# Kernel tuning notes

Hardware: AMD Instinct MI355X
Metric: run time of the kernel (lower is better)

Reference implementation:

```python
import jax, jax.numpy as jnp
import numpy as np

N, E, G = 20000, 320000, 64
IN_DIM, HID, HEADS, NCLS = 512, 256, 2, 10
EPS = 1e-5
SLOPE = 0.2


def setup_inputs() -> dict:
    key = jax.random.key(0)
    ks = jax.random.split(key, 24)
    s = 0.02
    inp = {
        "feat": jax.random.normal(ks[0], (N, IN_DIM), jnp.float32),
        "src": jax.random.randint(ks[1], (E,), 0, N, jnp.int32),
        "dst": jax.random.randint(ks[2], (E,), 0, N, jnp.int32),
        "graph_ids": jnp.sort(jax.random.randint(ks[3], (N,), 0, G, jnp.int32)),
        # GATv2Conv params (fc_src, fc_dst, attn)
        "W_src": jax.random.normal(ks[4], (IN_DIM, HEADS * HID), jnp.float32) * s,
        "b_src": jnp.zeros((HEADS * HID,), jnp.float32),
        "W_dst": jax.random.normal(ks[5], (IN_DIM, HEADS * HID), jnp.float32) * s,
        "b_dst": jnp.zeros((HEADS * HID,), jnp.float32),
        "attn": jax.random.normal(ks[6], (HEADS, HID), jnp.float32) * s,
        # skip_lin: input_dim -> 2*hidden
        "W_skip": jax.random.normal(ks[7], (IN_DIM, 2 * HID), jnp.float32) * s,
        "b_skip": jnp.zeros((2 * HID,), jnp.float32),
        # bn1 affine
        "gamma": jnp.ones((2 * HID,), jnp.float32),
        "beta": jnp.zeros((2 * HID,), jnp.float32),
        # dim_reducer
        "W_red": jax.random.normal(ks[8], (2 * HID, HID), jnp.float32) * s,
        "b_red": jnp.zeros((HID,), jnp.float32),
        # attention-pool gate Linear(hidden, 1)
        "w_gate": jax.random.normal(ks[9], (HID, 1), jnp.float32) * s,
        "b_gate": jnp.zeros((1,), jnp.float32),
        # classifier MLP
        "W1": jax.random.normal(ks[10], (HID, HID // 2), jnp.float32) * s,
        "b1": jnp.zeros((HID // 2,), jnp.float32),
        "W2": jax.random.normal(ks[11], (HID // 2, NCLS), jnp.float32) * s,
        "b2": jnp.zeros((NCLS,), jnp.float32),
    }
    return inp


def _gatv2(feat, src, dst, W_src, b_src, W_dst, b_dst, attn):
    # feat_src/feat_dst: [N, H, D]
    fs = (feat @ W_src + b_src).reshape(N, HEADS, HID)
    fd = (feat @ W_dst + b_dst).reshape(N, HEADS, HID)
    fs_e = fs[src]                               # [E, H, D]
    m = jax.nn.leaky_relu(fs_e + fd[dst], SLOPE)  # [E, H, D]
    e = jnp.einsum("ehd,hd->eh", m, attn)         # [E, H]
    # edge softmax grouped by destination node
    e_max = jax.ops.segment_max(e, dst, num_segments=N)          # [N, H]
    e_exp = jnp.exp(e - e_max[dst])                               # [E, H]
    denom = jax.ops.segment_sum(e_exp, dst, num_segments=N)      # [N, H]
    alpha = e_exp / denom[dst]                                    # [E, H]
    out = jax.ops.segment_sum(alpha[:, :, None] * fs_e, dst, num_segments=N)
    return out  # [N, H, D]; zero rows for zero in-degree nodes


def reference(feat, src, dst, graph_ids, W_src, b_src, W_dst, b_dst, attn,
              W_skip, b_skip, gamma, beta, W_red, b_red, w_gate, b_gate,
              W1, b1, W2, b2):
    h1 = jax.nn.elu(_gatv2(feat, src, dst, W_src, b_src, W_dst, b_dst, attn))
    h1 = h1.reshape(N, HEADS * HID)
    h1 = h1 + (feat @ W_skip + b_skip)
    # BatchNorm1d (training-mode batch statistics, biased variance)
    mu = jnp.mean(h1, axis=0)
    var = jnp.mean((h1 - mu) ** 2, axis=0)
    h1 = (h1 - mu) * jax.lax.rsqrt(var + EPS) * gamma + beta
    hr = h1 @ W_red + b_red                      # [N, HID]
    # GlobalAttentionPooling: segment softmax of gate scores over each graph
    gate = hr @ w_gate + b_gate                  # [N, 1]
    g_max = jax.ops.segment_max(gate, graph_ids, num_segments=G)
    g_exp = jnp.exp(gate - g_max[graph_ids])
    g_den = jax.ops.segment_sum(g_exp, graph_ids, num_segments=G)
    a = g_exp / g_den[graph_ids]                 # [N, 1]
    h_g = jax.ops.segment_sum(a * hr, graph_ids, num_segments=G)  # [G, HID]
    # classifier (dropout = identity at inference)
    return jax.nn.relu(h_g @ W1 + b1) @ W2 + b2  # [G, NCLS]
```

## Files before the change

kernel.cpp:

```cpp
#include <hip/hip_runtime.h>
#include <math.h>

#define N_NODES 20000
#define N_EDGES 320000
#define N_GRAPH 64
#define IN_DIM  512
#define HID     256
#define F2      512
#define EPS_BN  1e-5f
#define SLOPE   0.2f
#define SCAN_BLOCKS 79
#define N_RT    157
#define RT_PAD  20096

#define SF_BLOCKS   5024
#define SW_BLOCKS   1024
#define INIT_BLOCKS 79
#define HIST_BLOCKS 1250
#define PREP_BLOCKS (SF_BLOCKS + SW_BLOCKS + INIT_BLOCKS + HIST_BLOCKS)
#define TRIPLE_BLOCKS 1920

typedef unsigned short u16;
typedef __attribute__((ext_vector_type(8))) short bf16x8;
typedef __attribute__((ext_vector_type(4))) float floatx4;
typedef _Float16 f16;
typedef __attribute__((ext_vector_type(2))) f16 f16x2;

__device__ __forceinline__ u16 bf_hi(float x) {
    unsigned int u = __float_as_uint(x);
    return (u16)((u + 0x7fffu + ((u >> 16) & 1u)) >> 16);
}
__device__ __forceinline__ float bf_val(u16 h) {
    return __uint_as_float((unsigned int)h << 16);
}
__device__ __forceinline__ f16x2 h2_from_u32(unsigned int u) {
    return __builtin_bit_cast(f16x2, u);
}
__device__ __forceinline__ unsigned int u32_from_h2(f16x2 h) {
    return __builtin_bit_cast(unsigned int, h);
}

__device__ __forceinline__ void gload16(const u16* g, u16* l) {
    __builtin_amdgcn_global_load_lds(
        (const __attribute__((address_space(1))) void*)g,
        (__attribute__((address_space(3))) void*)l, 16, 0, 0);
}

__global__ __launch_bounds__(256) void prep_kernel(
    const float* __restrict__ feat, u16* __restrict__ Fhi,
    const float* __restrict__ Ws, const float* __restrict__ Wd,
    const float* __restrict__ Wk, const float* __restrict__ Wr,
    u16* __restrict__ Whi, u16* __restrict__ Wlo,
    const int* __restrict__ dst, int* __restrict__ counts,
    int* __restrict__ cursor,
    float* __restrict__ stats, float* __restrict__ h_gnum,
    float* __restrict__ gden) {
    __shared__ float t[32][33];
    int b = blockIdx.x;
    int tid = threadIdx.x;
    if (b < SF_BLOCKS) {
        int i = b * 256 + tid;
        size_t base = (size_t)i * 8;
        if (i >= N_NODES * IN_DIM / 8) {
            *(uint4*)(Fhi + base) = make_uint4(0, 0, 0, 0);
            return;
        }
        float4 x0 = *(const float4*)(feat + base);
        float4 x1 = *(const float4*)(feat + base + 4);
        float xs[8] = {x0.x, x0.y, x0.z, x0.w, x1.x, x1.y, x1.z, x1.w};
        union { u16 s[8]; uint4 v; } h;
#pragma unroll
        for (int j = 0; j < 8; j++) h.s[j] = bf_hi(xs[j]);
        *(uint4*)(Fhi + base) = h.v;
    } else if (b < SF_BLOCKS + SW_BLOCKS) {
        int bb = b - SF_BLOCKS;
        int kx = bb & 15, ny = (bb >> 4) & 15, w = bb >> 8;
        int ncols = (w == 3) ? 256 : 512;
        int n0 = ny * 32;
        if (n0 >= ncols) return;
        const float* W = (w == 0) ? Ws : ((w == 1) ? Wd : ((w == 2) ? Wk : Wr));
        size_t obase = (size_t)w * 512 * 512;
        int k0 = kx * 32;
        int tx = tid & 31, ty = tid >> 5;
#pragma unroll
        for (int i = 0; i < 4; i++)
            t[ty * 4 + i][tx] = W[(size_t)(k0 + ty * 4 + i) * ncols + n0 + tx];
        __syncthreads();
#pragma unroll
        for (int i = 0; i < 4; i++) {
            float x = t[tx][ty * 4 + i];
            u16 hh = bf_hi(x);
            size_t o = obase + (size_t)(n0 + ty * 4 + i) * 512 + k0 + tx;
            Whi[o] = hh;
            Wlo[o] = bf_hi(x - bf_val(hh));
        }
    } else if (b < SF_BLOCKS + SW_BLOCKS + INIT_BLOCKS) {
        int i = (b - SF_BLOCKS - SW_BLOCKS) * 256 + tid;
        if (i < N_NODES) cursor[i] = 0;
        if (i < 1024) stats[i] = 0.f;
        if (i < N_GRAPH * HID) h_gnum[i] = 0.f;
        if (i < N_GRAPH) gden[i] = 0.f;
    } else {
        int e = (b - SF_BLOCKS - SW_BLOCKS - INIT_BLOCKS) * 256 + tid;
        if (e < N_EDGES) atomicAdd(&counts[dst[e]], 1);
    }
}

__global__ __launch_bounds__(256) void gemm_mfma_triple(
    const u16* __restrict__ Fhi, const u16* __restrict__ Wthi,
    const float* __restrict__ b_src, const float* __restrict__ b_dst,
    const float* __restrict__ b_skip,
    u16* __restrict__ FS16, u16* __restrict__ FD16,
    u16* __restrict__ h1hi, u16* __restrict__ h1lo,
    const int* __restrict__ counts, int* __restrict__ row_ptr,
    int* __restrict__ bsum) {
    __shared__ u16 S[2][2][8192];
    int b = blockIdx.x;
    int tid = threadIdx.x;
    if (b >= TRIPLE_BLOCKS) {
        int* buf = (int*)&S[0][0][0];
        int bb = b - TRIPLE_BLOCKS;
        int i = bb * 256 + tid;
        buf[tid] = (i < N_NODES) ? counts[i] : 0;
        __syncthreads();
        for (int off = 1; off < 256; off <<= 1) {
            int t = (tid >= off) ? buf[tid - off] : 0;
            __syncthreads();
            buf[tid] += t;
            __syncthreads();
        }
        if (i < N_NODES) row_ptr[i + 1] = buf[tid];
        if (tid == 255) bsum[bb] = buf[255];
        return;
    }
    int xcd = b & 7, slot = b >> 3;
    int rt = (slot / 12) * 8 + xcd;
    if (rt >= N_RT) return;
    int cw = slot % 12;
    int w_idx = cw >> 2;
    int col0 = (cw & 3) * 128;
    int row0 = rt * 128;
    int lane = tid & 63, wave = tid >> 6;
    int wm = (wave & 1) * 64, wn = (wave >> 1) * 64;
    int quad = lane >> 4, l16 = lane & 15;

    int lrow = lane >> 3;
    int kswz = ((lane & 7) ^ lrow) << 3;
    const u16* aS = Fhi + (size_t)(row0 + wave * 32 + lrow) * 512 + kswz;
    const u16* bS = Wthi + (size_t)w_idx * 512 * 512 +
                    (size_t)(col0 + wave * 32 + lrow) * 512 + kswz;

#define STAGE(buf, kk)                                                        \
    do {                                                                      \
        gload16(aS + (size_t)(kk) * 64,         &S[buf][0][(wave * 4 + 0) * 512]); \
        gload16(bS + (size_t)(kk) * 64,         &S[buf][1][(wave * 4 + 0) * 512]); \
        gload16(aS + 4096 + (size_t)(kk) * 64,  &S[buf][0][(wave * 4 + 1) * 512]); \
        gload16(bS + 4096 + (size_t)(kk) * 64,  &S[buf][1][(wave * 4 + 1) * 512]); \
        gload16(aS + 8192 + (size_t)(kk) * 64,  &S[buf][0][(wave * 4 + 2) * 512]); \
        gload16(bS + 8192 + (size_t)(kk) * 64,  &S[buf][1][(wave * 4 + 2) * 512]); \
        gload16(aS + 12288 + (size_t)(kk) * 64, &S[buf][0][(wave * 4 + 3) * 512]); \
        gload16(bS + 12288 + (size_t)(kk) * 64, &S[buf][1][(wave * 4 + 3) * 512]); \
    } while (0)

    int kx8 = (l16 & 7) << 3;
    int oS0 = (quad * 8) ^ kx8;
    int offA = (wm + l16) * 64;
    int offB = (wn + l16) * 64;

    floatx4 acc[4][4];
#pragma unroll
    for (int i = 0; i < 4; i++)
#pragma unroll
        for (int j = 0; j < 4; j++) acc[i][j] = (floatx4){0.f, 0.f, 0.f, 0.f};

    STAGE(0, 0);
    __syncthreads();

#pragma unroll
    for (int kk = 0; kk < 8; kk++) {
        if (kk < 7) STAGE((kk + 1) & 1, kk + 1);
        const u16* A = &S[kk & 1][0][0];
        const u16* B = &S[kk & 1][1][0];
        bf16x8 bv[4][2];
#pragma unroll
        for (int nt = 0; nt < 4; nt++) {
            bv[nt][0] = *(const bf16x8*)&B[offB + nt * 1024 + oS0];
            bv[nt][1] = *(const bf16x8*)&B[offB + nt * 1024 + (oS0 ^ 32)];
        }
#pragma unroll
        for (int mt = 0; mt < 4; mt++) {
            bf16x8 a0 = *(const bf16x8*)&A[offA + mt * 1024 + oS0];
            bf16x8 a1 = *(const bf16x8*)&A[offA + mt * 1024 + (oS0 ^ 32)];
#pragma unroll
            for (int nt = 0; nt < 4; nt++) {
                acc[mt][nt] = __builtin_amdgcn_mfma_f32_16x16x32_bf16(
                    bv[nt][0], a0, acc[mt][nt], 0, 0, 0);
                acc[mt][nt] = __builtin_amdgcn_mfma_f32_16x16x32_bf16(
                    bv[nt][1], a1, acc[mt][nt], 0, 0, 0);
            }
        }
        __syncthreads();
    }
#undef STAGE

    const float* bias = (w_idx == 0) ? b_src : ((w_idx == 1) ? b_dst : b_skip);
    float4 b4[4];
#pragma unroll
    for (int wt = 0; wt < 4; wt++)
        b4[wt] = *(const float4*)(bias + col0 + wn + wt * 16 + quad * 4);

    u16* C = &S[0][0][0];
#pragma unroll
    for (int ft = 0; ft < 4; ft++) {
        int r = wm + ft * 16 + l16;
        int rx = r & 7;
#pragma unroll
        for (int wt = 0; wt < 4; wt++) {
            int cb = wn + wt * 16 + quad * 4;
            int off = r * 128 + (((cb >> 3) ^ rx) << 3) + (cb & 4);
            float v0 = acc[ft][wt][0] + b4[wt].x;
            float v1 = acc[ft][wt][1] + b4[wt].y;
            float v2 = acc[ft][wt][2] + b4[wt].z;
            float v3 = acc[ft][wt][3] + b4[wt].w;
            if (w_idx <= 1) {
                f16x2 p0; p0[0] = (f16)v0; p0[1] = (f16)v1;
                f16x2 p1; p1[0] = (f16)v2; p1[1] = (f16)v3;
                uint2 wv;
                wv.x = u32_from_h2(p0);
                wv.y = u32_from_h2(p1);
                *(uint2*)&C[off] = wv;
            } else {
                u16 h0 = bf_hi(v0), h1_ = bf_hi(v1), h2 = bf_hi(v2), h3 = bf_hi(v3);
                uint2 wv;
                wv.x = (unsigned)h0 | ((unsigned)h1_ << 16);
                wv.y = (unsigned)h2 | ((unsigned)h3 << 16);
                *(uint2*)&C[off] = wv;
                uint2 lv;
                lv.x = (unsigned)bf_hi(v0 - bf_val(h0)) | ((unsigned)bf_hi(v1 - bf_val(h1_)) << 16);
                lv.y = (unsigned)bf_hi(v2 - bf_val(h2)) | ((unsigned)bf_hi(v3 - bf_val(h3)) << 16);
                *(uint2*)&C[16384 + off] = lv;
            }
        }
    }
    __syncthreads();
    {
        int tr = tid >> 4;
        int tc = tid & 15;
        u16* outp = (w_idx == 0) ? FS16 : ((w_idx == 1) ? FD16 : h1hi);
#pragma unroll
        for (int i = 0; i < 8; i++) {
            int r = i * 16 + tr;
            int m = row0 + r;
            int loff = r * 128 + ((tc ^ (r & 7)) << 3);
            uint4 v = *(const uint4*)&C[loff];
            if (m < N_NODES) {
                *(uint4*)(outp + (size_t)m * 512 + col0 + tc * 8) = v;
                if (w_idx == 2) {
                    uint4 vl = *(const uint4*)&C[16384 + loff];
                    *(uint4*)(h1lo + (size_t)m * 512 + col0 + tc * 8) = vl;
                }
            }
        }
    }
}

__global__ __launch_bounds__(256) void scan_fixup_kernel(
    const int* __restrict__ bsum, int* __restrict__ row_ptr) {
    __shared__ int red[256];
    int b = blockIdx.x, tid = threadIdx.x;
    red[tid] = (tid < b) ? bsum[tid] : 0;
    __syncthreads();
    for (int off = 128; off > 0; off >>= 1) {
        if (tid < off) red[tid] += red[tid + off];
        __syncthreads();
    }
    int offset = red[0];
    int i = b * 256 + tid;
    if (i < N_NODES) row_ptr[i + 1] += offset;
    if (b == 0 && tid == 0) row_ptr[0] = 0;
}

__global__ void scatter_kernel(const int* __restrict__ src, const int* __restrict__ dst,
                               const int* __restrict__ row_ptr,
                               int* __restrict__ cursor, int* __restrict__ csr_src) {
    int e = blockIdx.x * blockDim.x + threadIdx.x;
    if (e < N_EDGES) {
        int d = dst[e];
        int pos = atomicAdd(&cursor[d], 1);
        csr_src[row_ptr[d] + pos] = src[e];
    }
}

__global__ __launch_bounds__(256) void edge_fused_kernel(
    const u16* __restrict__ FS16, const u16* __restrict__ FD16,
    const float* __restrict__ attn, const int* __restrict__ csr_src,
    const int* __restrict__ row_ptr,
    u16* __restrict__ h1hi, u16* __restrict__ h1lo) {
    int tid = threadIdx.x;
    int lane = tid & 63, wave = tid >> 6;
    int n = blockIdx.x * 4 + wave;
    int beg = row_ptr[n], end = row_ptr[n + 1];

    f16x2 fd2[4], aw2[4];
    {
        uint4 q = *(const uint4*)(FD16 + (size_t)n * 512 + 8 * lane);
        fd2[0] = h2_from_u32(q.x); fd2[1] = h2_from_u32(q.y);
        fd2[2] = h2_from_u32(q.z); fd2[3] = h2_from_u32(q.w);
        float4 a0 = *(const float4*)(attn + 8 * lane);
        float4 a1 = *(const float4*)(attn + 8 * lane + 4);
        aw2[0][0] = (f16)a0.x; aw2[0][1] = (f16)a0.y;
        aw2[1][0] = (f16)a0.z; aw2[1][1] = (f16)a0.w;
        aw2[2][0] = (f16)a1.x; aw2[2][1] = (f16)a1.y;
        aw2[3][0] = (f16)a1.z; aw2[3][1] = (f16)a1.w;
    }

    const f16x2 sl2 = {(f16)SLOPE, (f16)SLOPE};
    float acc[8] = {0.f, 0.f, 0.f, 0.f, 0.f, 0.f, 0.f, 0.f};
    float den = 0.f;
    const u16* FSb = FS16 + 8 * lane;

    int j = beg;
    for (; j + 3 < end; j += 4) {
        int s0 = csr_src[j];
        int s1 = csr_src[j + 1];
        int s2 = csr_src[j + 2];
        int s3 = csr_src[j + 3];
        uint4 q0 = *(const uint4*)(FSb + (size_t)s0 * 512);
        uint4 q1 = *(const uint4*)(FSb + (size_t)s1 * 512);
        uint4 q2 = *(const uint4*)(FSb + (size_t)s2 * 512);
        uint4 q3 = *(const uint4*)(FSb + (size_t)s3 * 512);
        f16x2 f0[4], f1[4], f2[4], f3[4];
        f0[0] = h2_from_u32(q0.x); f0[1] = h2_from_u32(q0.y);
        f0[2] = h2_from_u32(q0.z); f0[3] = h2_from_u32(q0.w);
        f1[0] = h2_from_u32(q1.x); f1[1] = h2_from_u32(q1.y);
        f1[2] = h2_from_u32(q1.z); f1[3] = h2_from_u32(q1.w);
        f2[0] = h2_from_u32(q2.x); f2[1] = h2_from_u32(q2.y);
        f2[2] = h2_from_u32(q2.z); f2[3] = h2_from_u32(q2.w);
        f3[0] = h2_from_u32(q3.x); f3[1] = h2_from_u32(q3.y);
        f3[2] = h2_from_u32(q3.z); f3[3] = h2_from_u32(q3.w);
        float p0 = 0.f, p1 = 0.f, p2 = 0.f, p3 = 0.f;
#pragma unroll
        for (int k = 0; k < 4; k++) {
            f16x2 sm0 = f0[k] + fd2[k];
            p0 = __builtin_amdgcn_fdot2(
                __builtin_elementwise_max(sm0, sm0 * sl2), aw2[k], p0, false);
            f16x2 sm1 = f1[k] + fd2[k];
            p1 = __builtin_amdgcn_fdot2(
                __builtin_elementwise_max(sm1, sm1 * sl2), aw2[k], p1, false);
            f16x2 sm2 = f2[k] + fd2[k];
            p2 = __builtin_amdgcn_fdot2(
                __builtin_elementwise_max(sm2, sm2 * sl2), aw2[k], p2, false);
            f16x2 sm3 = f3[k] + fd2[k];
            p3 = __builtin_amdgcn_fdot2(
                __builtin_elementwise_max(sm3, sm3 * sl2), aw2[k], p3, false);
        }
#pragma unroll
        for (int off = 16; off > 0; off >>= 1) {
            p0 += __shfl_xor(p0, off, 64);
            p1 += __shfl_xor(p1, off, 64);
            p2 += __shfl_xor(p2, off, 64);
            p3 += __shfl_xor(p3, off, 64);
        }
        float e0 = __expf(p0);
        float e1 = __expf(p1);
        float e2 = __expf(p2);
        float e3 = __expf(p3);
#pragma unroll
        for (int k = 0; k < 4; k++) {
            acc[2 * k]     += e0 * (float)f0[k][0] + e1 * (float)f1[k][0]
                            + e2 * (float)f2[k][0] + e3 * (float)f3[k][0];
            acc[2 * k + 1] += e0 * (float)f0[k][1] + e1 * (float)f1[k][1]
                            + e2 * (float)f2[k][1] + e3 * (float)f3[k][1];
        }
        den += (e0 + e1) + (e2 + e3);
    }
    for (; j < end; j++) {
        int s = csr_src[j];
        uint4 q = *(const uint4*)(FSb + (size_t)s * 512);
        f16x2 f2v[4];
        f2v[0] = h2_from_u32(q.x); f2v[1] = h2_from_u32(q.y);
        f2v[2] = h2_from_u32(q.z); f2v[3] = h2_from_u32(q.w);
        float p = 0.f;
#pragma unroll
        for (int k = 0; k < 4; k++) {
            f16x2 sm = f2v[k] + fd2[k];
            p = __builtin_amdgcn_fdot2(
                __builtin_elementwise_max(sm, sm * sl2), aw2[k], p, false);
        }
#pragma unroll
        for (int off = 16; off > 0; off >>= 1) p += __shfl_xor(p, off, 64);
        float ex = __expf(p);
#pragma unroll
        for (int k = 0; k < 4; k++) {
            acc[2 * k]     += ex * (float)f2v[k][0];
            acc[2 * k + 1] += ex * (float)f2v[k][1];
        }
        den += ex;
    }

    float inv = den > 0.f ? 1.f / den : 0.f;
    size_t base = (size_t)n * 512 + 8 * lane;
    union { u16 s[8]; uint4 v; } qh, ql;
    qh.v = *(const uint4*)(h1hi + base);
    ql.v = *(const uint4*)(h1lo + base);
#pragma unroll
    for (int k = 0; k < 8; k++) {
        float skip = bf_val(qh.s[k]) + bf_val(ql.s[k]);
        float x = acc[k] * inv;
        x = x > 0.f ? x : expm1f(x);
        float y = x + skip;
        u16 hh = bf_hi(y);
        qh.s[k] = hh;
        ql.s[k] = bf_hi(y - bf_val(hh));
    }
    *(uint4*)(h1hi + base) = qh.v;
    *(uint4*)(h1lo + base) = ql.v;
}

__global__ __launch_bounds__(256) void bn_stats_kernel(const u16* __restrict__ h1hi,
                                                       float* __restrict__ stats,
                                                       int rows_per_block) {
    int tid = threadIdx.x;
    int r0 = blockIdx.x * rows_per_block;
    int r1 = min(r0 + rows_per_block, N_NODES);
    float s0 = 0.f, q0 = 0.f, s1 = 0.f, q1 = 0.f;
    for (int r = r0; r < r1; r++) {
        float a = bf_val(h1hi[(size_t)r * F2 + tid]);
        float b = bf_val(h1hi[(size_t)r * F2 + 256 + tid]);
        s0 += a; q0 += a * a;
        s1 += b; q1 += b * b;
    }
    atomicAdd(&stats[tid], s0);
    atomicAdd(&stats[256 + tid], s1);
    atomicAdd(&stats[512 + tid], q0);
    atomicAdd(&stats[512 + 256 + tid], q1);
}

__global__ __launch_bounds__(256) void bn_fold_kernel(
    const float* __restrict__ stats, const float* __restrict__ gamma,
    const float* __restrict__ beta,
    const u16* __restrict__ Whi3, const u16* __restrict__ Wlo3,
    const float* __restrict__ b_red,
    u16* __restrict__ Wphi, u16* __restrict__ Wplo, float* __restrict__ bias2) {
    __shared__ float sScale[512], sShift[512];
    __shared__ float red[256];
    int n = blockIdx.x, tid = threadIdx.x;
    for (int c = tid; c < 512; c += 256) {
        float mu = stats[c] / (float)N_NODES;
        float var = stats[512 + c] / (float)N_NODES - mu * mu;
        float sc = gamma[c] * rsqrtf(var + EPS_BN);
        sScale[c] = sc;
        sShift[c] = beta[c] - mu * sc;
    }
    __syncthreads();
    float part = 0.f;
    for (int k = tid; k < 512; k += 256) {
        size_t o = (size_t)n * 512 + k;
        float w = bf_val(Whi3[o]) + bf_val(Wlo3[o]);
        part += sShift[k] * w;
        float wp = w * sScale[k];
        u16 hh = bf_hi(wp);
        Wphi[o] = hh;
        Wplo[o] = bf_hi(wp - bf_val(hh));
    }
    red[tid] = part; __syncthreads();
    for (int off = 128; off > 0; off >>= 1) {
        if (tid < off) red[tid] += red[tid + off];
        __syncthreads();
    }
    if (tid == 0) bias2[n] = b_red[n] + red[0];
}

__global__ __launch_bounds__(512) void gemm_mfma_red(
    const u16* __restrict__ Ahi, const u16* __restrict__ Alo,
    const u16* __restrict__ Bhi, const u16* __restrict__ Blo,
    const float* __restrict__ bias2, const float* __restrict__ wg,
    const int* __restrict__ gids,
    float* __restrict__ h_gnum, float* __restrict__ gden) {
    __shared__ u16 AsHi[128 * 40];
    __shared__ u16 AsLo[128 * 40];
    __shared__ float gacc[128];
    __shared__ float pacc[8][256];
    __shared__ float dacc[8];
    int tid = threadIdx.x;
    int row0 = blockIdx.x * 128;
    int lane = tid & 63, wave = tid >> 6;
    int wm = (wave & 1) * 64, wn = (wave >> 1) * 64;
    int quad = lane >> 4, l16 = lane & 15;

    if (tid < 128) gacc[tid] = 0.f;
    if (tid < 8) dacc[tid] = 0.f;
    for (int i = tid; i < 8 * 256; i += 512) ((float*)pacc)[i] = 0.f;

    int sr = tid >> 2, sh = (tid & 3) * 8;
    int grow = row0 + sr;
    bool ok = grow < N_NODES;
    u16* sH = &AsHi[sr * 40 + sh];
    u16* sL = &AsLo[sr * 40 + sh];

    const u16* bPh[4];
    const u16* bPl[4];
#pragma unroll
    for (int nt = 0; nt < 4; nt++) {
        size_t o = (size_t)(wn + nt * 16 + l16) * 512 + quad * 8;
        bPh[nt] = Bhi + o;
        bPl[nt] = Blo + o;
    }

    floatx4 acc[4][4];
#pragma unroll
    for (int i = 0; i < 4; i++)
#pragma unroll
        for (int j = 0; j < 4; j++) acc[i][j] = (floatx4){0.f, 0.f, 0.f, 0.f};

    for (int k0 = 0; k0 < 512; k0 += 32) {
        uint4 h0 = make_uint4(0, 0, 0, 0), l0 = h0;
        if (ok) {
            h0 = *(const uint4*)(Ahi + (size_t)grow * 512 + k0 + sh);
            l0 = *(const uint4*)(Alo + (size_t)grow * 512 + k0 + sh);
        }
        union { uint4 u; bf16x8 v; } bh[4], bl[4];
#pragma unroll
        for (int nt = 0; nt < 4; nt++) {
            bh[nt].u = *(const uint4*)(bPh[nt] + k0);
            bl[nt].u = *(const uint4*)(bPl[nt] + k0);
        }
        __syncthreads();
        *(uint4*)sH = h0;
        *(uint4*)sL = l0;
        __syncthreads();
#pragma unroll
        for (int mt = 0; mt < 4; mt++) {
            int me = (wm + mt * 16 + l16) * 40 + quad * 8;
            bf16x8 ah = *(const bf16x8*)&AsHi[me];
            bf16x8 al = *(const bf16x8*)&AsLo[me];
#pragma unroll
            for (int nt = 0; nt < 4; nt++) {
                acc[mt][nt] = __builtin_amdgcn_mfma_f32_16x16x32_bf16(bh[nt].v, ah, acc[mt][nt], 0, 0, 0);
                acc[mt][nt] = __builtin_amdgcn_mfma_f32_16x16x32_bf16(bl[nt].v, ah, acc[mt][nt], 0, 0, 0);
                acc[mt][nt] = __builtin_amdgcn_mfma_f32_16x16x32_bf16(bh[nt].v, al, acc[mt][nt], 0, 0, 0);
            }
        }
    }

    float4 b4[4], w4[4];
#pragma unroll
    for (int wt = 0; wt < 4; wt++) {
        int nb = wn + wt * 16 + quad * 4;
        b4[wt] = *(const float4*)(bias2 + nb);
        w4[wt] = *(const float4*)(wg + nb);
    }
#pragma unroll
    for (int ft = 0; ft < 4; ft++) {
        int r = wm + ft * 16 + l16;
        float g = 0.f;
#pragma unroll
        for (int wt = 0; wt < 4; wt++) {
            float4 v;
            v.x = acc[ft][wt][0] + b4[wt].x;
            v.y = acc[ft][wt][1] + b4[wt].y;
            v.z = acc[ft][wt][2] + b4[wt].z;
            v.w = acc[ft][wt][3] + b4[wt].w;
            g += v.x * w4[wt].x + v.y * w4[wt].y + v.z * w4[wt].z + v.w * w4[wt].w;
        }
        g += __shfl_xor(g, 16, 64);
        g += __shfl_xor(g, 32, 64);
        if (quad == 0) atomicAdd(&gacc[r], g);
    }
    __syncthreads();

    int g0 = gids[row0];
#pragma unroll
    for (int ft = 0; ft < 4; ft++) {
        int r = wm + ft * 16 + l16;
        int m = row0 + r;
        if (m >= N_NODES) continue;
        float wgt = __expf(gacc[r]);
        int d = gids[m] - g0;
        if (d < 8) {
            if ((wave >> 1) == 0 && quad == 0) atomicAdd(&dacc[d], wgt);
#pragma unroll
            for (int wt = 0; wt < 4; wt++) {
                int nb = wn + wt * 16 + quad * 4;
                atomicAdd(&pacc[d][nb + 0], wgt * (acc[ft][wt][0] + b4[wt].x));
                atomicAdd(&pacc[d][nb + 1], wgt * (acc[ft][wt][1] + b4[wt].y));
                atomicAdd(&pacc[d][nb + 2], wgt * (acc[ft][wt][2] + b4[wt].z));
                atomicAdd(&pacc[d][nb + 3], wgt * (acc[ft][wt][3] + b4[wt].w));
            }
        } else {
            int gg = gids[m];
            if ((wave >> 1) == 0 && quad == 0) atomicAdd(&gden[gg], wgt);
#pragma unroll
            for (int wt = 0; wt < 4; wt++) {
                int nb = wn + wt * 16 + quad * 4;
                atomicAdd(&h_gnum[gg * HID + nb + 0], wgt * (acc[ft][wt][0] + b4[wt].x));
                atomicAdd(&h_gnum[gg * HID + nb + 1], wgt * (acc[ft][wt][1] + b4[wt].y));
                atomicAdd(&h_gnum[gg * HID + nb + 2], wgt * (acc[ft][wt][2] + b4[wt].z));
                atomicAdd(&h_gnum[gg * HID + nb + 3], wgt * (acc[ft][wt][3] + b4[wt].w));
            }
        }
    }
    __syncthreads();

    int mlast = min(row0 + 127, N_NODES - 1);
    int span = gids[mlast] - g0;
    if (span > 7) span = 7;
    for (int i = tid; i < (span + 1) * 256; i += 512) {
        int d = i >> 8, c = i & 255;
        atomicAdd(&h_gnum[(g0 + d) * HID + c], pacc[d][c]);
    }
    if (tid <= span) atomicAdd(&gden[g0 + tid], dacc[tid]);
}

__global__ __launch_bounds__(128) void classifier_kernel(
    const float* __restrict__ h_gnum, const float* __restrict__ gden,
    const float* __restrict__ W1, const float* __restrict__ b1,
    const float* __restrict__ W2, const float* __restrict__ b2,
    float* __restrict__ out) {
    int g = blockIdx.x;
    int tid = threadIdx.x;
    __shared__ float hg[256];
    __shared__ float z1[128];
    float d = gden[g];
    float invd = d > 0.f ? 1.f / d : 0.f;
    hg[tid] = h_gnum[g * HID + tid] * invd;
    hg[tid + 128] = h_gnum[g * HID + tid + 128] * invd;
    __syncthreads();
    float a = b1[tid];
#pragma unroll 8
    for (int k = 0; k < 256; k++) a += hg[k] * W1[k * 128 + tid];
    z1[tid] = a > 0.f ? a : 0.f;
    __syncthreads();
    if (tid < 10) {
        float o = b2[tid];
#pragma unroll 8
        for (int j = 0; j < 128; j++) o += z1[j] * W2[j * 10 + tid];
        out[g * 10 + tid] = o;
    }
}

extern "C" void kernel_launch(void* const* d_in, const int* in_sizes, int n_in,
                              void* d_out, int out_size, void* d_ws, size_t ws_size,
                              hipStream_t stream) {
    const float* feat   = (const float*)d_in[0];
    const int*   src    = (const int*)d_in[1];
    const int*   dst    = (const int*)d_in[2];
    const int*   gids   = (const int*)d_in[3];
    const float* W_src  = (const float*)d_in[4];
    const float* b_src  = (const float*)d_in[5];
    const float* W_dst  = (const float*)d_in[6];
    const float* b_dst  = (const float*)d_in[7];
    const float* attn   = (const float*)d_in[8];
    const float* W_skip = (const float*)d_in[9];
    const float* b_skip = (const float*)d_in[10];
    const float* gamma  = (const float*)d_in[11];
    const float* beta   = (const float*)d_in[12];
    const float* W_red  = (const float*)d_in[13];
    const float* b_red  = (const float*)d_in[14];
    const float* w_gate = (const float*)d_in[15];
    const float* W1     = (const float*)d_in[17];
    const float* b1     = (const float*)d_in[18];
    const float* W2     = (const float*)d_in[19];
    const float* b2     = (const float*)d_in[20];
    float* out = (float*)d_out;

    char* p = (char*)d_ws;
    auto alloc = [&](size_t bytes) -> char* {
        char* r = p;
        p += (bytes + 255) & ~(size_t)255;
        return r;
    };
    u16*   FS16     = (u16*)alloc((size_t)N_NODES * F2 * 2);
    u16*   FD16     = (u16*)alloc((size_t)N_NODES * F2 * 2);
    u16*   h1hi     = (u16*)alloc((size_t)N_NODES * F2 * 2);
    u16*   h1lo     = (u16*)alloc((size_t)N_NODES * F2 * 2);
    float* stats    = (float*)alloc(1024 * 4);
    float* bias2    = (float*)alloc(256 * 4);
    float* h_gnum   = (float*)alloc((size_t)N_GRAPH * HID * 4);
    float* gden     = (float*)alloc((size_t)N_GRAPH * 4);
    int* counts     = (int*)alloc((size_t)N_NODES * 4);
    int* row_ptr    = (int*)alloc((size_t)(N_NODES + 1) * 4);
    int* cursor     = (int*)alloc((size_t)N_NODES * 4);
    int* csr_src    = (int*)alloc((size_t)N_EDGES * 4);
    int* bsum       = (int*)alloc((size_t)SCAN_BLOCKS * 4);
    u16* Fhi        = (u16*)alloc((size_t)RT_PAD * IN_DIM * 2);
    u16* Wthi       = (u16*)alloc((size_t)4 * 512 * 512 * 2);
    u16* Wtlo       = (u16*)alloc((size_t)4 * 512 * 512 * 2);
    u16* Wphi       = (u16*)alloc((size_t)HID * 512 * 2);
    u16* Wplo       = (u16*)alloc((size_t)HID * 512 * 2);
    (void)ws_size; (void)in_sizes; (void)n_in; (void)out_size;

    const size_t WSZ = (size_t)512 * 512;

    hipMemsetAsync(counts, 0, (size_t)N_NODES * 4, stream);

    prep_kernel<<<PREP_BLOCKS, 256, 0, stream>>>(
        feat, Fhi, W_src, W_dst, W_skip, W_red, Wthi, Wtlo,
        dst, counts, cursor, stats, h_gnum, gden);

    gemm_mfma_triple<<<TRIPLE_BLOCKS + SCAN_BLOCKS, 256, 0, stream>>>(
        Fhi, Wthi, b_src, b_dst, b_skip, FS16, FD16, h1hi, h1lo,
        counts, row_ptr, bsum);

    scan_fixup_kernel<<<SCAN_BLOCKS, 256, 0, stream>>>(bsum, row_ptr);
    scatter_kernel<<<(N_EDGES + 255) / 256, 256, 0, stream>>>(src, dst, row_ptr, cursor, csr_src);

    edge_fused_kernel<<<N_NODES / 4, 256, 0, stream>>>(
        FS16, FD16, attn, csr_src, row_ptr, h1hi, h1lo);

    bn_stats_kernel<<<500, 256, 0, stream>>>(h1hi, stats, 40);
    bn_fold_kernel<<<HID, 256, 0, stream>>>(
        stats, gamma, beta, Wthi + 3 * WSZ, Wtlo + 3 * WSZ, b_red, Wphi, Wplo, bias2);

    gemm_mfma_red<<<N_RT, 512, 0, stream>>>(
        h1hi, h1lo, Wphi, Wplo, bias2, w_gate, gids, h_gnum, gden);

    classifier_kernel<<<N_GRAPH, 128, 0, stream>>>(h_gnum, gden, W1, b1, W2, b2, out);
}
```

Before: 390.9 us.

## Double-buffer reduction GEMM with direct global-to-LDS loads and smaller row tiles

```diff
diff --git a/kernel.cpp b/kernel.cpp
--- a/kernel.cpp
+++ b/kernel.cpp
@@ -11,6 +11,7 @@
 #define SLOPE   0.2f
 #define SCAN_BLOCKS 79
 #define N_RT    157
+#define N_RT2   313
 #define RT_PAD  20096
 
 #define SF_BLOCKS   5024
@@ -471,32 +472,30 @@
     if (tid == 0) bias2[n] = b_red[n] + red[0];
 }
 
-__global__ __launch_bounds__(512) void gemm_mfma_red(
+__global__ __launch_bounds__(256) void gemm_mfma_red(
     const u16* __restrict__ Ahi, const u16* __restrict__ Alo,
     const u16* __restrict__ Bhi, const u16* __restrict__ Blo,
     const float* __restrict__ bias2, const float* __restrict__ wg,
     const int* __restrict__ gids,
     float* __restrict__ h_gnum, float* __restrict__ gden) {
-    __shared__ u16 AsHi[128 * 40];
-    __shared__ u16 AsLo[128 * 40];
-    __shared__ float gacc[128];
+    __shared__ u16 AS[2][2][64 * 32];
+    __shared__ float gacc[64];
     __shared__ float pacc[8][256];
     __shared__ float dacc[8];
     int tid = threadIdx.x;
-    int row0 = blockIdx.x * 128;
+    int row0 = blockIdx.x * 64;
     int lane = tid & 63, wave = tid >> 6;
-    int wm = (wave & 1) * 64, wn = (wave >> 1) * 64;
+    int wn = wave * 64;
     int quad = lane >> 4, l16 = lane & 15;
 
-    if (tid < 128) gacc[tid] = 0.f;
+    if (tid < 64) gacc[tid] = 0.f;
     if (tid < 8) dacc[tid] = 0.f;
-    for (int i = tid; i < 8 * 256; i += 512) ((float*)pacc)[i] = 0.f;
-
-    int sr = tid >> 2, sh = (tid & 3) * 8;
-    int grow = row0 + sr;
-    bool ok = grow < N_NODES;
-    u16* sH = &AsHi[sr * 40 + sh];
-    u16* sL = &AsLo[sr * 40 + sh];
+    for (int i = tid; i < 8 * 256; i += 256) ((float*)pacc)[i] = 0.f;
+
+    int arow = wave * 16 + (lane >> 2);
+    int aoff = (lane & 3) * 8;
+    const u16* aH = Ahi + (size_t)(row0 + arow) * 512 + aoff;
+    const u16* aL = Alo + (size_t)(row0 + arow) * 512 + aoff;
 
     const u16* bPh[4];
     const u16* bPl[4];
@@ -513,35 +512,47 @@
 #pragma unroll
         for (int j = 0; j < 4; j++) acc[i][j] = (floatx4){0.f, 0.f, 0.f, 0.f};
 
-    for (int k0 = 0; k0 < 512; k0 += 32) {
-        uint4 h0 = make_uint4(0, 0, 0, 0), l0 = h0;
-        if (ok) {
-            h0 = *(const uint4*)(Ahi + (size_t)grow * 512 + k0 + sh);
-            l0 = *(const uint4*)(Alo + (size_t)grow * 512 + k0 + sh);
-        }
-        union { uint4 u; bf16x8 v; } bh[4], bl[4];
-#pragma unroll
-        for (int nt = 0; nt < 4; nt++) {
-            bh[nt].u = *(const uint4*)(bPh[nt] + k0);
-            bl[nt].u = *(const uint4*)(bPl[nt] + k0);
+#define ASTAGE(buf, kk)                                   \
+    do {                                                  \
+        gload16(aH + (kk) * 32, &AS[buf][0][wave * 512]); \
+        gload16(aL + (kk) * 32, &AS[buf][1][wave * 512]); \
+    } while (0)
+
+    union { uint4 u; bf16x8 v; } bh[2][4], bl[2][4];
+    ASTAGE(0, 0);
+#pragma unroll
+    for (int nt = 0; nt < 4; nt++) {
+        bh[0][nt].u = *(const uint4*)(bPh[nt]);
+        bl[0][nt].u = *(const uint4*)(bPl[nt]);
+    }
+    __syncthreads();
+
+#pragma unroll
+    for (int k = 0; k < 16; k++) {
+        int cb = k & 1;
+        if (k < 15) {
+            ASTAGE(cb ^ 1, k + 1);
+#pragma unroll
+            for (int nt = 0; nt < 4; nt++) {
+                bh[cb ^ 1][nt].u = *(const uint4*)(bPh[nt] + (k + 1) * 32);
+                bl[cb ^ 1][nt].u = *(const uint4*)(bPl[nt] + (k + 1) * 32);
+            }
+        }
+#pragma unroll
+        for (int mt = 0; mt < 4; mt++) {
+            int me = (mt * 16 + l16) * 32 + quad * 8;
+            bf16x8 ah = *(const bf16x8*)&AS[cb][0][me];
+            bf16x8 al = *(const bf16x8*)&AS[cb][1][me];
+#pragma unroll
+            for (int nt = 0; nt < 4; nt++) {
+                acc[mt][nt] = __builtin_amdgcn_mfma_f32_16x16x32_bf16(bh[cb][nt].v, ah, acc[mt][nt], 0, 0, 0);
+                acc[mt][nt] = __builtin_amdgcn_mfma_f32_16x16x32_bf16(bl[cb][nt].v, ah, acc[mt][nt], 0, 0, 0);
+                acc[mt][nt] = __builtin_amdgcn_mfma_f32_16x16x32_bf16(bh[cb][nt].v, al, acc[mt][nt], 0, 0, 0);
+            }
         }
         __syncthreads();
-        *(uint4*)sH = h0;
-        *(uint4*)sL = l0;
-        __syncthreads();
-#pragma unroll
-        for (int mt = 0; mt < 4; mt++) {
-            int me = (wm + mt * 16 + l16) * 40 + quad * 8;
-            bf16x8 ah = *(const bf16x8*)&AsHi[me];
-            bf16x8 al = *(const bf16x8*)&AsLo[me];
-#pragma unroll
-            for (int nt = 0; nt < 4; nt++) {
-                acc[mt][nt] = __builtin_amdgcn_mfma_f32_16x16x32_bf16(bh[nt].v, ah, acc[mt][nt], 0, 0, 0);
-                acc[mt][nt] = __builtin_amdgcn_mfma_f32_16x16x32_bf16(bl[nt].v, ah, acc[mt][nt], 0, 0, 0);
-                acc[mt][nt] = __builtin_amdgcn_mfma_f32_16x16x32_bf16(bh[nt].v, al, acc[mt][nt], 0, 0, 0);
-            }
-        }
-    }
+    }
+#undef ASTAGE
 
     float4 b4[4], w4[4];
 #pragma unroll
@@ -552,7 +563,7 @@
     }
 #pragma unroll
     for (int ft = 0; ft < 4; ft++) {
-        int r = wm + ft * 16 + l16;
+        int r = ft * 16 + l16;
         float g = 0.f;
 #pragma unroll
         for (int wt = 0; wt < 4; wt++) {
@@ -572,13 +583,13 @@
     int g0 = gids[row0];
 #pragma unroll
     for (int ft = 0; ft < 4; ft++) {
-        int r = wm + ft * 16 + l16;
+        int r = ft * 16 + l16;
         int m = row0 + r;
         if (m >= N_NODES) continue;
         float wgt = __expf(gacc[r]);
         int d = gids[m] - g0;
         if (d < 8) {
-            if ((wave >> 1) == 0 && quad == 0) atomicAdd(&dacc[d], wgt);
+            if (wave == 0 && quad == 0) atomicAdd(&dacc[d], wgt);
 #pragma unroll
             for (int wt = 0; wt < 4; wt++) {
                 int nb = wn + wt * 16 + quad * 4;
@@ -589,7 +600,7 @@
             }
         } else {
             int gg = gids[m];
-            if ((wave >> 1) == 0 && quad == 0) atomicAdd(&gden[gg], wgt);
+            if (wave == 0 && quad == 0) atomicAdd(&gden[gg], wgt);
 #pragma unroll
             for (int wt = 0; wt < 4; wt++) {
                 int nb = wn + wt * 16 + quad * 4;
@@ -602,10 +613,10 @@
     }
     __syncthreads();
 
-    int mlast = min(row0 + 127, N_NODES - 1);
+    int mlast = min(row0 + 63, N_NODES - 1);
     int span = gids[mlast] - g0;
     if (span > 7) span = 7;
-    for (int i = tid; i < (span + 1) * 256; i += 512) {
+    for (int i = tid; i < (span + 1) * 256; i += 256) {
         int d = i >> 8, c = i & 255;
         atomicAdd(&h_gnum[(g0 + d) * HID + c], pacc[d][c]);
     }
@@ -712,7 +723,7 @@
     bn_fold_kernel<<<HID, 256, 0, stream>>>(
         stats, gamma, beta, Wthi + 3 * WSZ, Wtlo + 3 * WSZ, b_red, Wphi, Wplo, bias2);
 
-    gemm_mfma_red<<<N_RT, 512, 0, stream>>>(
+    gemm_mfma_red<<<N_RT2, 256, 0, stream>>>(
         h1hi, h1lo, Wphi, Wplo, bias2, w_gate, gids, h_gnum, gden);
 
     classifier_kernel<<<N_GRAPH, 128, 0, stream>>>(h_gnum, gden, W1, b1, W2, b2, out);
```

After: 402.4 us. +2.9%, slower.
